# Optimization experiments

Measured on AMD Instinct MI355X. Metric: run time of the kernel, lower is better.

Reference implementation:

```python
import jax, jax.numpy as jnp
import numpy as np

D, N, L, H, VOCAB = 256, 8192, 6, 4, 256
EPS = 1e-5


def layernorm(x):
    # LayerNorm over last dim, no affine (matches nn.LayerNorm(D, elementwise_affine=False))
    mu = jnp.mean(x, axis=-1, keepdims=True)
    var = jnp.mean(jnp.square(x - mu), axis=-1, keepdims=True)
    return (x - mu) * jax.lax.rsqrt(var + EPS)


def rotate_half(x):
    x1, x2 = jnp.split(x, 2, axis=-1)
    return jnp.concatenate((-x2, x1), axis=-1)


def rope_tables(T, dim, dtype):
    inv_freq = 1.0 / (10000.0 ** (jnp.arange(0, dim, 2, dtype=jnp.float32) / dim))
    t = jnp.arange(T, dtype=jnp.float32)
    freqs = jnp.einsum('i,j->ij', t, inv_freq)          # [T, dim/2]
    emb = jnp.concatenate((freqs, freqs), axis=-1)       # [T, dim]
    return jnp.cos(emb).astype(dtype), jnp.sin(emb).astype(dtype)


def linear_attention(Q, K, V):
    # unnormalized causal attention with RoPE on Q, K
    B, T, d = Q.shape
    cos, sin = rope_tables(T, d, Q.dtype)
    Qr = Q * cos + rotate_half(Q) * sin
    Kr = K * cos + rotate_half(K) * sin
    energy = jnp.einsum('btd,bsd->bts', Qr, Kr)          # [B, T, T]
    mask = jnp.tril(jnp.ones((T, T), dtype=energy.dtype))
    energy = energy * mask
    return jnp.einsum('bts,bsd->btd', energy, V)


def setup_inputs() -> dict:
    key = jax.random.key(0)
    ks = jax.random.split(key, 6)
    idx = jax.random.randint(ks[0], (4, 2048), 0, VOCAB)
    wte = jax.random.normal(ks[1], (VOCAB, D), dtype=jnp.float32) * 0.02
    encoder = jax.random.normal(ks[2], (N, D), dtype=jnp.float32) * 0.02
    decoder_x = jax.random.normal(ks[3], (H, D, N // H), dtype=jnp.float32) * 0.02
    decoder_y = jax.random.normal(ks[4], (H, D, N // H), dtype=jnp.float32) * 0.02
    readout = jax.random.normal(ks[5], (D, VOCAB), dtype=jnp.float32) * 0.02
    return {"idx": idx, "wte": wte, "encoder": encoder,
            "decoder_x": decoder_x, "decoder_y": decoder_y, "readout": readout}


def reference(idx, wte, encoder, decoder_x, decoder_y, readout):
    B, T = idx.shape
    v_ast = layernorm(wte[idx])                          # [B, T, D]
    for _ in range(L):
        x_raw = jnp.einsum('btd,hdm->bthm', v_ast, decoder_x)
        x = jax.nn.relu(x_raw)                           # [B, T, H, N/H]
        a_ast = linear_attention(v_ast, v_ast, v_ast)
        y_raw = jnp.einsum('btd,hdm->bthm', layernorm(a_ast), decoder_y)
        y = jax.nn.relu(y_raw) * x
        y_flat = y.reshape(B, T, -1)                     # [B, T, N]
        update = y_flat @ encoder                        # [B, T, D]
        v_ast = v_ast + layernorm(update)
    logits = v_ast @ readout                             # [B, T, VOCAB]
    return logits
```

## Files before the change

### kernel.cpp

```cpp
#include <hip/hip_runtime.h>
#include <hip/hip_bf16.h>

typedef __hip_bfloat16 bf16;
typedef _Float16 half_t;
typedef __attribute__((ext_vector_type(8))) _Float16 half8;
typedef __attribute__((ext_vector_type(4))) float f32x4;

#define LN_EPS 1e-5f

static constexpr int Dk     = 256;
static constexpr int Tk     = 2048;
static constexpr int BTk    = 8192;
static constexpr int MHk    = 2048;
static constexpr int Nk     = 8192;
static constexpr int LAYERS = 6;
static constexpr long long TD  = (long long)Tk * Dk;
static constexpr long long BTD = (long long)BTk * Dk;
static constexpr long long TT  = (long long)Tk * Tk;

#define SKQ(t) ((((t) & 3) ^ (((t) >> 3) & 3)) * 8)

__device__ __forceinline__ float wave_reduce(float v) {
#pragma unroll
    for (int o = 32; o > 0; o >>= 1) v += __shfl_down(v, o);
    return v;
}

__device__ __forceinline__ float block_sum_256(float x, float* sbuf) {
    float s = wave_reduce(x);
    int lane = threadIdx.x & 63, wv = threadIdx.x >> 6;
    if (lane == 0) sbuf[wv] = s;
    __syncthreads();
    float r = sbuf[0] + sbuf[1] + sbuf[2] + sbuf[3];
    __syncthreads();
    return r;
}

__device__ __forceinline__ void glds16(const void* g, void* lds) {
    __builtin_amdgcn_global_load_lds(
        (const __attribute__((address_space(1))) void*)g,
        (__attribute__((address_space(3))) void*)lds, 16, 0, 0);
}

__global__ __launch_bounds__(256) void sniff_kernel(const unsigned short* __restrict__ w,
                                                    int* __restrict__ flag) {
    __shared__ float sbuf[4];
    int tid = threadIdx.x;
    float cnt = 0.f;
    for (int i = tid; i < 1024; i += 256) {
        int e = (w[i] >> 7) & 0xFF;
        if (e >= 128) cnt += 1.f;
    }
    float tot = block_sum_256(cnt, sbuf);
    if (tid == 0) *flag = (tot > 32.f) ? 1 : 0;
}

__global__ __launch_bounds__(256) void tr_cvt16_kernel(const void* __restrict__ src,
                                                       const int* __restrict__ flag,
                                                       half_t* __restrict__ dst,
                                                       int R, int C,
                                                       long long sz, long long dz) {
    __shared__ float t[32][33];
    bool f32 = (*flag != 0);
    int ct = blockIdx.x * 32, rt = blockIdx.y * 32;
    long long so = (long long)blockIdx.z * sz, dofs = (long long)blockIdx.z * dz;
    int tx = threadIdx.x & 31, ty = threadIdx.x >> 5;
#pragma unroll
    for (int i = 0; i < 4; i++) {
        long long idx = so + (long long)(rt + ty + i * 8) * C + ct + tx;
        t[ty + i * 8][tx] = f32 ? ((const float*)src)[idx] : (float)((const bf16*)src)[idx];
    }
    __syncthreads();
#pragma unroll
    for (int i = 0; i < 4; i++) {
        long long odx = dofs + (long long)(ct + ty + i * 8) * R + rt + tx;
        dst[odx] = (half_t)t[tx][ty + i * 8];
    }
}

__global__ __launch_bounds__(256) void trv_kernel(const float* __restrict__ src,
                                                  half_t* __restrict__ dst) {
    __shared__ float t[32][33];
    int ct = blockIdx.x * 32, rt = blockIdx.y * 32;
    int tx = threadIdx.x & 31, ty = threadIdx.x >> 5;
#pragma unroll
    for (int i = 0; i < 4; i++)
        t[ty + i * 8][tx] = src[(long long)(rt + ty + i * 8) * Dk + ct + tx];
    __syncthreads();
#pragma unroll
    for (int i = 0; i < 4; i++)
        dst[(long long)(ct + ty + i * 8) * BTk + rt + tx] = (half_t)t[tx][ty + i * 8];
}

__global__ __launch_bounds__(256) void embed_ln_kernel(const int* __restrict__ idx,
                                                       const void* __restrict__ wte,
                                                       const int* __restrict__ flag,
                                                       float* __restrict__ v,
                                                       half_t* __restrict__ vf) {
    __shared__ float sbuf[4];
    int bt = blockIdx.x, tid = threadIdx.x;
    int id = idx[bt];
    bool f32 = (*flag != 0);
    float x = f32 ? ((const float*)wte)[id * Dk + tid]
                  : (float)((const bf16*)wte)[id * Dk + tid];
    float mu = block_sum_256(x, sbuf) * (1.f / 256.f);
    float d = x - mu;
    float var = block_sum_256(d * d, sbuf) * (1.f / 256.f);
    float r = d * rsqrtf(var + LN_EPS);
    v[bt * Dk + tid] = r;
    vf[bt * Dk + tid] = (half_t)r;
}

__global__ __launch_bounds__(256) void ln_rows_kernel(const float* __restrict__ Pa,
                                                      half_t* __restrict__ of) {
    __shared__ float sbuf[4];
    int bt = blockIdx.x, tid = threadIdx.x;
    int b = bt >> 11, t = bt & (Tk - 1);
    int ncnt = ((t & ~127) >> 9) + 1;
    const float* p = Pa + ((long long)(b << 2)) * TD + (long long)t * Dk + tid;
    float x = 0.f;
    for (int c = 0; c < ncnt; c++) x += p[(long long)c * TD];
    float mu = block_sum_256(x, sbuf) * (1.f / 256.f);
    float d = x - mu;
    float var = block_sum_256(d * d, sbuf) * (1.f / 256.f);
    float r = d * rsqrtf(var + LN_EPS);
    of[bt * Dk + tid] = (half_t)r;
}

__global__ __launch_bounds__(256) void add_ln_kernel(const float* __restrict__ Pu,
                                                     float* __restrict__ v,
                                                     half_t* __restrict__ vf) {
    __shared__ float sbuf[4];
    int bt = blockIdx.x, tid = threadIdx.x;
    long long e = (long long)bt * Dk + tid;
    float x = Pu[e] + Pu[e + BTD] + Pu[e + 2 * BTD] + Pu[e + 3 * BTD];
    float mu = block_sum_256(x, sbuf) * (1.f / 256.f);
    float d = x - mu;
    float var = block_sum_256(d * d, sbuf) * (1.f / 256.f);
    float r = d * rsqrtf(var + LN_EPS);
    float nv = v[e] + r;
    v[e] = nv;
    vf[e] = (half_t)nv;
}

__global__ __launch_bounds__(128) void rope_kernel(const float* __restrict__ v,
                                                   half_t* __restrict__ qf) {
    int bt = blockIdx.x, i = threadIdx.x;
    int t = bt & (Tk - 1);
    float invf = powf(10000.f, -(float)i / 128.f);
    float ang = (float)t * invf;
    float s, c;
    sincosf(ang, &s, &c);
    float q1 = v[bt * Dk + i];
    float q2 = v[bt * Dk + 128 + i];
    qf[bt * Dk + i]       = (half_t)(q1 * c - q2 * s);
    qf[bt * Dk + 128 + i] = (half_t)(q2 * c + q1 * s);
}

__global__ __launch_bounds__(256) void gemm128e(
    const half_t* __restrict__ Q, half_t* __restrict__ E) {
    __shared__ __align__(16) half_t smem[8192];
    half_t* As = smem;
    half_t* Bs = smem + 4096;
    const int tid = threadIdx.x;
    const int lane = tid & 63, wv = tid >> 6;
    const int wr = wv >> 1, wc = wv & 1;
    const int quad = lane >> 4, r = lane & 15;
    const int qsw = (quad ^ ((r >> 1) & 3)) * 8;
    const int mb = blockIdx.y * 128, nb = blockIdx.x * 128;
    if ((int)blockIdx.x > (int)blockIdx.y) return;
    const half_t* Qb = Q + (long long)blockIdx.z * TD;
    half_t* Eb = E + (long long)blockIdx.z * TT;

    f32x4 acc[4][4] = {};
    const int srow = tid >> 2, skq = SKQ(tid);
    const int wbase = (tid & 192) * 8;
    for (int k0 = 0; k0 < Dk; k0 += 32) {
#pragma unroll
        for (int rnd = 0; rnd < 2; rnd++) {
            int row = rnd * 64 + srow;
            glds16(Qb + (long long)(mb + row) * Dk + k0 + skq, As + rnd * 2048 + wbase);
            glds16(Qb + (long long)(nb + row) * Dk + k0 + skq, Bs + rnd * 2048 + wbase);
        }
        __syncthreads();
        half8 bfr[4];
#pragma unroll
        for (int ni = 0; ni < 4; ni++)
            bfr[ni] = *(const half8*)&Bs[(wc * 64 + ni * 16 + r) * 32 + qsw];
#pragma unroll
        for (int mi = 0; mi < 4; mi++) {
            half8 afr = *(const half8*)&As[(wr * 64 + mi * 16 + r) * 32 + qsw];
#pragma unroll
            for (int ni = 0; ni < 4; ni++)
                acc[mi][ni] = __builtin_amdgcn_mfma_f32_16x16x32_f16(afr, bfr[ni], acc[mi][ni], 0, 0, 0);
        }
        __syncthreads();
    }
#pragma unroll
    for (int p = 0; p < 2; p++) {
        if (wr == p) {
#pragma unroll
            for (int mi = 0; mi < 4; mi++)
#pragma unroll
                for (int ni = 0; ni < 4; ni++) {
                    int rl0 = mi * 16 + quad * 4;
                    int cl = wc * 64 + ni * 16 + r;
#pragma unroll
                    for (int rr = 0; rr < 4; rr++) {
                        int row = mb + p * 64 + rl0 + rr;
                        int col = nb + cl;
                        float val = (row < col) ? 0.f : acc[mi][ni][rr];
                        smem[(rl0 + rr) * 128 + cl] = (half_t)val;
                    }
                }
        }
        __syncthreads();
#pragma unroll
        for (int j = 0; j < 4; j++) {
            int o = j * 2048 + tid * 8;
            int rl = o >> 7, cl = o & 127;
            *(half8*)&Eb[(long long)(mb + p * 64 + rl) * Tk + nb + cl] = *(const half8*)&smem[o];
        }
        __syncthreads();
    }
}

__global__ __launch_bounds__(256) void gemm128a(
    const half_t* __restrict__ E, const half_t* __restrict__ vT,
    float* __restrict__ Pa) {
    __shared__ __align__(16) half_t As[128 * 32];
    __shared__ __align__(16) half_t Bs[128 * 32];
    const int tid = threadIdx.x;
    const int lane = tid & 63, wv = tid >> 6;
    const int wr = wv >> 1, wc = wv & 1;
    const int quad = lane >> 4, r = lane & 15;
    const int qsw = (quad ^ ((r >> 1) & 3)) * 8;
    const int mb = blockIdx.y * 128, nb = blockIdx.x * 128;
    const int b = blockIdx.z >> 2, c = blockIdx.z & 3;
    const int kbeg = c * 512;
    const int kend = min(mb + 128, kbeg + 512);
    if (kend <= kbeg) return;

    const half_t* Ab = E + (long long)b * TT;
    const half_t* Bb = vT + (long long)b * Tk;
    float* Pc = Pa + (long long)blockIdx.z * TD;
    f32x4 acc[4][4] = {};
    const int srow = tid >> 2, skq = SKQ(tid);
    const int wbase = (tid & 192) * 8;
    for (int k0 = kbeg; k0 < kend; k0 += 32) {
#pragma unroll
        for (int rnd = 0; rnd < 2; rnd++) {
            int row = rnd * 64 + srow;
            glds16(Ab + (long long)(mb + row) * Tk + k0 + skq, As + rnd * 2048 + wbase);
            glds16(Bb + (long long)(nb + row) * BTk + k0 + skq, Bs + rnd * 2048 + wbase);
        }
        __syncthreads();
        half8 bfr[4];
#pragma unroll
        for (int ni = 0; ni < 4; ni++)
            bfr[ni] = *(const half8*)&Bs[(wc * 64 + ni * 16 + r) * 32 + qsw];
#pragma unroll
        for (int mi = 0; mi < 4; mi++) {
            half8 afr = *(const half8*)&As[(wr * 64 + mi * 16 + r) * 32 + qsw];
#pragma unroll
            for (int ni = 0; ni < 4; ni++)
                acc[mi][ni] = __builtin_amdgcn_mfma_f32_16x16x32_f16(afr, bfr[ni], acc[mi][ni], 0, 0, 0);
        }
        __syncthreads();
    }
#pragma unroll
    for (int mi = 0; mi < 4; mi++)
#pragma unroll
        for (int ni = 0; ni < 4; ni++) {
            int row0 = mb + wr * 64 + mi * 16 + quad * 4;
            int col = nb + wc * 64 + ni * 16 + r;
#pragma unroll
            for (int rr = 0; rr < 4; rr++)
                Pc[(long long)(row0 + rr) * Dk + col] = acc[mi][ni][rr];
        }
}

__global__ __launch_bounds__(512) void dual_gemm(
    const half_t* __restrict__ A1,
    const half_t* __restrict__ A2,
    const half_t* __restrict__ dxT,
    const half_t* __restrict__ dyT,
    half_t* __restrict__ C) {
    __shared__ __align__(16) half_t smem[16384];
    half_t* As1 = smem;
    half_t* As2 = smem + 4096;
    half_t* Bs1 = smem + 8192;
    half_t* Bs2 = smem + 12288;
    const int tid = threadIdx.x;
    const int lane = tid & 63, wv = tid >> 6;
    const int wr = wv >> 2, wc = wv & 3;
    const int quad = lane >> 4, r = lane & 15;
    const int qsw = (quad ^ ((r >> 1) & 3)) * 8;
    const int mb = blockIdx.y * 128, nb = blockIdx.x * 128;
    const int h = blockIdx.z;
    const half_t* B1 = dxT + (long long)h * MHk * Dk;
    const half_t* B2 = dyT + (long long)h * MHk * Dk;

    f32x4 accX[4][2] = {};
    f32x4 accY[4][2] = {};
    const int srow = tid >> 2, skq = SKQ(tid);
    const int wbase = (tid & 448) * 8;
    for (int k0 = 0; k0 < Dk; k0 += 32) {
        glds16(A1 + (long long)(mb + srow) * Dk + k0 + skq, As1 + wbase);
        glds16(A2 + (long long)(mb + srow) * Dk + k0 + skq, As2 + wbase);
        glds16(B1 + (long long)(nb + srow) * Dk + k0 + skq, Bs1 + wbase);
        glds16(B2 + (long long)(nb + srow) * Dk + k0 + skq, Bs2 + wbase);
        __syncthreads();
        half8 b1f[2], b2f[2];
#pragma unroll
        for (int ni = 0; ni < 2; ni++) {
            b1f[ni] = *(const half8*)&Bs1[(wc * 32 + ni * 16 + r) * 32 + qsw];
            b2f[ni] = *(const half8*)&Bs2[(wc * 32 + ni * 16 + r) * 32 + qsw];
        }
#pragma unroll
        for (int mi = 0; mi < 4; mi++) {
            half8 a1 = *(const half8*)&As1[(wr * 64 + mi * 16 + r) * 32 + qsw];
            half8 a2 = *(const half8*)&As2[(wr * 64 + mi * 16 + r) * 32 + qsw];
#pragma unroll
            for (int ni = 0; ni < 2; ni++) {
                accX[mi][ni] = __builtin_amdgcn_mfma_f32_16x16x32_f16(a1, b1f[ni], accX[mi][ni], 0, 0, 0);
                accY[mi][ni] = __builtin_amdgcn_mfma_f32_16x16x32_f16(a2, b2f[ni], accY[mi][ni], 0, 0, 0);
            }
        }
        __syncthreads();
    }
#pragma unroll
    for (int mi = 0; mi < 4; mi++)
#pragma unroll
        for (int ni = 0; ni < 2; ni++) {
            int rl0 = wr * 64 + mi * 16 + quad * 4;
            int cl = wc * 32 + ni * 16 + r;
#pragma unroll
            for (int rr = 0; rr < 4; rr++) {
                float val = fmaxf(accY[mi][ni][rr], 0.f) * fmaxf(accX[mi][ni][rr], 0.f);
                smem[(rl0 + rr) * 128 + cl] = (half_t)val;
            }
        }
    __syncthreads();
    const long long cbase = (long long)mb * Nk + (long long)h * MHk + nb;
#pragma unroll
    for (int j = 0; j < 4; j++) {
        int o = j * 4096 + tid * 8;
        int rl = o >> 7, cl = o & 127;
        *(half8*)&C[cbase + (long long)rl * Nk + cl] = *(const half8*)&smem[o];
    }
}

__global__ __launch_bounds__(256) void gemm128u(
    const half_t* __restrict__ A, const half_t* __restrict__ B,
    float* __restrict__ Pu) {
    __shared__ __align__(16) half_t As[128 * 32];
    __shared__ __align__(16) half_t Bs[128 * 32];
    const int tid = threadIdx.x;
    const int lane = tid & 63, wv = tid >> 6;
    const int wr = wv >> 1, wc = wv & 1;
    const int quad = lane >> 4, r = lane & 15;
    const int qsw = (quad ^ ((r >> 1) & 3)) * 8;
    const int mb = blockIdx.y * 128, nb = blockIdx.x * 128;
    const int kbeg = blockIdx.z * 2048;
    float* Pc = Pu + (long long)blockIdx.z * BTD;

    f32x4 acc[4][4] = {};
    const int srow = tid >> 2, skq = SKQ(tid);
    const int wbase = (tid & 192) * 8;
    for (int k0 = kbeg; k0 < kbeg + 2048; k0 += 32) {
#pragma unroll
        for (int rnd = 0; rnd < 2; rnd++) {
            int row = rnd * 64 + srow;
            glds16(A + (long long)(mb + row) * Nk + k0 + skq, As + rnd * 2048 + wbase);
            glds16(B + (long long)(nb + row) * Nk + k0 + skq, Bs + rnd * 2048 + wbase);
        }
        __syncthreads();
        half8 bfr[4];
#pragma unroll
        for (int ni = 0; ni < 4; ni++)
            bfr[ni] = *(const half8*)&Bs[(wc * 64 + ni * 16 + r) * 32 + qsw];
#pragma unroll
        for (int mi = 0; mi < 4; mi++) {
            half8 afr = *(const half8*)&As[(wr * 64 + mi * 16 + r) * 32 + qsw];
#pragma unroll
            for (int ni = 0; ni < 4; ni++)
                acc[mi][ni] = __builtin_amdgcn_mfma_f32_16x16x32_f16(afr, bfr[ni], acc[mi][ni], 0, 0, 0);
        }
        __syncthreads();
    }
#pragma unroll
    for (int mi = 0; mi < 4; mi++)
#pragma unroll
        for (int ni = 0; ni < 4; ni++) {
            int row0 = mb + wr * 64 + mi * 16 + quad * 4;
            int col = nb + wc * 64 + ni * 16 + r;
#pragma unroll
            for (int rr = 0; rr < 4; rr++)
                Pc[(long long)(row0 + rr) * Dk + col] = acc[mi][ni][rr];
        }
}

__global__ __launch_bounds__(256) void gemm64h(
    const half_t* __restrict__ A, int lda,
    const half_t* __restrict__ B, int ldb,
    float* __restrict__ C, int ldc, int K) {
    __shared__ __align__(16) half_t As[64 * 32];
    __shared__ __align__(16) half_t Bs[64 * 32];
    const int tid = threadIdx.x;
    const int lane = tid & 63, wv = tid >> 6;
    const int wr = wv >> 1, wc = wv & 1;
    const int quad = lane >> 4, r = lane & 15;
    const int qsw = (quad ^ ((r >> 1) & 3)) * 8;
    const int mb = blockIdx.y * 64, nb = blockIdx.x * 64;

    f32x4 acc[2][2] = {};
    const int srow = tid >> 2, skq = SKQ(tid);
    const int wbase = (tid & 192) * 8;
    for (int k0 = 0; k0 < K; k0 += 32) {
        glds16(A + (long long)(mb + srow) * lda + k0 + skq, As + wbase);
        glds16(B + (long long)(nb + srow) * ldb + k0 + skq, Bs + wbase);
        __syncthreads();
        half8 b0 = *(const half8*)&Bs[(wc * 32 +  0 + r) * 32 + qsw];
        half8 b1 = *(const half8*)&Bs[(wc * 32 + 16 + r) * 32 + qsw];
#pragma unroll
        for (int mi = 0; mi < 2; mi++) {
            half8 afr = *(const half8*)&As[(wr * 32 + mi * 16 + r) * 32 + qsw];
            acc[mi][0] = __builtin_amdgcn_mfma_f32_16x16x32_f16(afr, b0, acc[mi][0], 0, 0, 0);
            acc[mi][1] = __builtin_amdgcn_mfma_f32_16x16x32_f16(afr, b1, acc[mi][1], 0, 0, 0);
        }
        __syncthreads();
    }
#pragma unroll
    for (int mi = 0; mi < 2; mi++)
#pragma unroll
        for (int ni = 0; ni < 2; ni++) {
            int row0 = mb + wr * 32 + mi * 16 + quad * 4;
            int col = nb + wc * 32 + ni * 16 + r;
#pragma unroll
            for (int rr = 0; rr < 4; rr++)
                C[(long long)(row0 + rr) * ldc + col] = acc[mi][ni][rr];
        }
}

extern "C" void kernel_launch(void* const* d_in, const int* in_sizes, int n_in,
                              void* d_out, int out_size, void* d_ws, size_t ws_size,
                              hipStream_t stream) {
    (void)in_sizes; (void)n_in; (void)out_size; (void)ws_size;
    const int* idx = (const int*)d_in[0];
    float* out = (float*)d_out;

    char* ws = (char*)d_ws;
    float*  v32  = (float*) (ws);
    half_t* vf   = (half_t*)(ws + (  8ll << 20));
    half_t* qf   = (half_t*)(ws + ( 12ll << 20));
    half_t* vT   = (half_t*)(ws + ( 16ll << 20));
    half_t* lnf  = (half_t*)(ws + ( 20ll << 20));
    half_t* E    = (half_t*)(ws + ( 24ll << 20));
    float*  Pa   = (float*) (ws + ( 56ll << 20));
    float*  Pu   = (float*) (ws + ( 24ll << 20));
    half_t* y16  = (half_t*)(ws + ( 88ll << 20));
    half_t* dxT  = (half_t*)(ws + (216ll << 20));
    half_t* dyT  = (half_t*)(ws + (220ll << 20));
    half_t* eT   = (half_t*)(ws + (224ll << 20));
    half_t* roT  = (half_t*)(ws + (228ll << 20));
    int*    flag = (int*)   (ws + (228ll << 20) + (256ll << 10));

    sniff_kernel<<<1, 256, 0, stream>>>((const unsigned short*)d_in[1], flag);
    tr_cvt16_kernel<<<dim3(MHk / 32, Dk / 32, 4), 256, 0, stream>>>(
        d_in[3], flag, dxT, Dk, MHk, (long long)Dk * MHk, (long long)Dk * MHk);
    tr_cvt16_kernel<<<dim3(MHk / 32, Dk / 32, 4), 256, 0, stream>>>(
        d_in[4], flag, dyT, Dk, MHk, (long long)Dk * MHk, (long long)Dk * MHk);
    tr_cvt16_kernel<<<dim3(Dk / 32, Nk / 32, 1), 256, 0, stream>>>(
        d_in[2], flag, eT, Nk, Dk, 0, 0);
    tr_cvt16_kernel<<<dim3(Dk / 32, Dk / 32, 1), 256, 0, stream>>>(
        d_in[5], flag, roT, Dk, Dk, 0, 0);

    embed_ln_kernel<<<BTk, 256, 0, stream>>>(idx, d_in[1], flag, v32, vf);

    for (int l = 0; l < LAYERS; l++) {
        rope_kernel<<<BTk, 128, 0, stream>>>(v32, qf);
        trv_kernel<<<dim3(Dk / 32, BTk / 32), 256, 0, stream>>>(v32, vT);
        gemm128e<<<dim3(Tk / 128, Tk / 128, 4), 256, 0, stream>>>(qf, E);
        gemm128a<<<dim3(Dk / 128, Tk / 128, 16), 256, 0, stream>>>(E, vT, Pa);
        ln_rows_kernel<<<BTk, 256, 0, stream>>>(Pa, lnf);
        dual_gemm<<<dim3(MHk / 128, BTk / 128, 4), 512, 0, stream>>>(
            vf, lnf, dxT, dyT, y16);
        gemm128u<<<dim3(Dk / 128, BTk / 128, 4), 256, 0, stream>>>(y16, eT, Pu);
        add_ln_kernel<<<BTk, 256, 0, stream>>>(Pu, v32, vf);
    }
    gemm64h<<<dim3(Dk / 64, BTk / 64), 256, 0, stream>>>(
        vf, Dk, roT, Dk, out, Dk, Dk);
}
```

Measured before the change: 1.450 ms.

## Fuse decoder dual GEMM with encoder GEMM, keeping gated activations in LDS

Replaces the separate dual_gemm (writing the fp16 y tensor to global memory) and gemm128u with one kernel. Each block computes a 128-row stripe of relu(x)*relu(y) for eight 128-column chunks, stores each chunk in swizzled LDS, and immediately multiplies it by the matching encoder slice, accumulating the update. Partial results from 8 N-splits are written out and summed in add_ln_kernel. This removes the large y16 round-trip through global memory and one launch. The cost is fewer blocks (512), much more LDS per block, and A-operand tiles reloaded for every chunk.

```diff
diff --git a/kernel.cpp b/kernel.cpp
--- a/kernel.cpp
+++ b/kernel.cpp
@@ -133,7 +133,9 @@
     __shared__ float sbuf[4];
     int bt = blockIdx.x, tid = threadIdx.x;
     long long e = (long long)bt * Dk + tid;
-    float x = Pu[e] + Pu[e + BTD] + Pu[e + 2 * BTD] + Pu[e + 3 * BTD];
+    float x = 0.f;
+#pragma unroll
+    for (int p = 0; p < 8; p++) x += Pu[e + (long long)p * BTD];
     float mu = block_sum_256(x, sbuf) * (1.f / 256.f);
     float d = x - mu;
     float var = block_sum_256(d * d, sbuf) * (1.f / 256.f);
@@ -280,124 +282,105 @@
         }
 }
 
-__global__ __launch_bounds__(512) void dual_gemm(
+__global__ __launch_bounds__(512, 2) void fused_du(
     const half_t* __restrict__ A1,
     const half_t* __restrict__ A2,
     const half_t* __restrict__ dxT,
     const half_t* __restrict__ dyT,
-    half_t* __restrict__ C) {
-    __shared__ __align__(16) half_t smem[16384];
-    half_t* As1 = smem;
-    half_t* As2 = smem + 4096;
-    half_t* Bs1 = smem + 8192;
-    half_t* Bs2 = smem + 12288;
+    const half_t* __restrict__ eT,
+    float* __restrict__ Pu) {
+    __shared__ __align__(16) half_t As1[4096];
+    __shared__ __align__(16) half_t As2[4096];
+    __shared__ __align__(16) half_t Bs1[4096];
+    __shared__ __align__(16) half_t Bs2[4096];
+    __shared__ __align__(16) half_t Ys[16384];
+    __shared__ __align__(16) half_t Es[8192];
     const int tid = threadIdx.x;
     const int lane = tid & 63, wv = tid >> 6;
     const int wr = wv >> 2, wc = wv & 3;
     const int quad = lane >> 4, r = lane & 15;
     const int qsw = (quad ^ ((r >> 1) & 3)) * 8;
-    const int mb = blockIdx.y * 128, nb = blockIdx.x * 128;
-    const int h = blockIdx.z;
-    const half_t* B1 = dxT + (long long)h * MHk * Dk;
-    const half_t* B2 = dyT + (long long)h * MHk * Dk;
-
-    f32x4 accX[4][2] = {};
-    f32x4 accY[4][2] = {};
+    const int mb = blockIdx.y * 128;
+    const int nbase = blockIdx.x * 1024;
     const int srow = tid >> 2, skq = SKQ(tid);
     const int wbase = (tid & 448) * 8;
-    for (int k0 = 0; k0 < Dk; k0 += 32) {
-        glds16(A1 + (long long)(mb + srow) * Dk + k0 + skq, As1 + wbase);
-        glds16(A2 + (long long)(mb + srow) * Dk + k0 + skq, As2 + wbase);
-        glds16(B1 + (long long)(nb + srow) * Dk + k0 + skq, Bs1 + wbase);
-        glds16(B2 + (long long)(nb + srow) * Dk + k0 + skq, Bs2 + wbase);
-        __syncthreads();
-        half8 b1f[2], b2f[2];
-#pragma unroll
-        for (int ni = 0; ni < 2; ni++) {
-            b1f[ni] = *(const half8*)&Bs1[(wc * 32 + ni * 16 + r) * 32 + qsw];
-            b2f[ni] = *(const half8*)&Bs2[(wc * 32 + ni * 16 + r) * 32 + qsw];
-        }
-#pragma unroll
-        for (int mi = 0; mi < 4; mi++) {
-            half8 a1 = *(const half8*)&As1[(wr * 64 + mi * 16 + r) * 32 + qsw];
-            half8 a2 = *(const half8*)&As2[(wr * 64 + mi * 16 + r) * 32 + qsw];
+
+    f32x4 accU[4][4] = {};
+    for (int nc = 0; nc < 8; nc++) {
+        const int n0 = nbase + nc * 128;
+        f32x4 accX[4][2] = {};
+        f32x4 accY[4][2] = {};
+        for (int k0 = 0; k0 < Dk; k0 += 32) {
+            glds16(A1 + (long long)(mb + srow) * Dk + k0 + skq, As1 + wbase);
+            glds16(A2 + (long long)(mb + srow) * Dk + k0 + skq, As2 + wbase);
+            glds16(dxT + (long long)(n0 + srow) * Dk + k0 + skq, Bs1 + wbase);
+            glds16(dyT + (long long)(n0 + srow) * Dk + k0 + skq, Bs2 + wbase);
+            __syncthreads();
+            half8 b1f[2], b2f[2];
 #pragma unroll
             for (int ni = 0; ni < 2; ni++) {
-                accX[mi][ni] = __builtin_amdgcn_mfma_f32_16x16x32_f16(a1, b1f[ni], accX[mi][ni], 0, 0, 0);
-                accY[mi][ni] = __builtin_amdgcn_mfma_f32_16x16x32_f16(a2, b2f[ni], accY[mi][ni], 0, 0, 0);
+                b1f[ni] = *(const half8*)&Bs1[(wc * 32 + ni * 16 + r) * 32 + qsw];
+                b2f[ni] = *(const half8*)&Bs2[(wc * 32 + ni * 16 + r) * 32 + qsw];
             }
-        }
-        __syncthreads();
-    }
-#pragma unroll
-    for (int mi = 0; mi < 4; mi++)
-#pragma unroll
-        for (int ni = 0; ni < 2; ni++) {
-            int rl0 = wr * 64 + mi * 16 + quad * 4;
-            int cl = wc * 32 + ni * 16 + r;
-#pragma unroll
-            for (int rr = 0; rr < 4; rr++) {
-                float val = fmaxf(accY[mi][ni][rr], 0.f) * fmaxf(accX[mi][ni][rr], 0.f);
-                smem[(rl0 + rr) * 128 + cl] = (half_t)val;
+#pragma unroll
+            for (int mi = 0; mi < 4; mi++) {
+                half8 a1 = *(const half8*)&As1[(wr * 64 + mi * 16 + r) * 32 + qsw];
+                half8 a2 = *(const half8*)&As2[(wr * 64 + mi * 16 + r) * 32 + qsw];
+#pragma unroll
+                for (int ni = 0; ni < 2; ni++) {
+                    accX[mi][ni] = __builtin_amdgcn_mfma_f32_16x16x32_f16(a1, b1f[ni], accX[mi][ni], 0, 0, 0);
+                    accY[mi][ni] = __builtin_amdgcn_mfma_f32_16x16x32_f16(a2, b2f[ni], accY[mi][ni], 0, 0, 0);
+                }
             }
-        }
-    __syncthreads();
-    const long long cbase = (long long)mb * Nk + (long long)h * MHk + nb;
-#pragma unroll
-    for (int j = 0; j < 4; j++) {
-        int o = j * 4096 + tid * 8;
-        int rl = o >> 7, cl = o & 127;
-        *(half8*)&C[cbase + (long long)rl * Nk + cl] = *(const half8*)&smem[o];
-    }
-}
-
-__global__ __launch_bounds__(256) void gemm128u(
-    const half_t* __restrict__ A, const half_t* __restrict__ B,
-    float* __restrict__ Pu) {
-    __shared__ __align__(16) half_t As[128 * 32];
-    __shared__ __align__(16) half_t Bs[128 * 32];
-    const int tid = threadIdx.x;
-    const int lane = tid & 63, wv = tid >> 6;
-    const int wr = wv >> 1, wc = wv & 1;
-    const int quad = lane >> 4, r = lane & 15;
-    const int qsw = (quad ^ ((r >> 1) & 3)) * 8;
-    const int mb = blockIdx.y * 128, nb = blockIdx.x * 128;
-    const int kbeg = blockIdx.z * 2048;
-    float* Pc = Pu + (long long)blockIdx.z * BTD;
-
-    f32x4 acc[4][4] = {};
-    const int srow = tid >> 2, skq = SKQ(tid);
-    const int wbase = (tid & 192) * 8;
-    for (int k0 = kbeg; k0 < kbeg + 2048; k0 += 32) {
-#pragma unroll
-        for (int rnd = 0; rnd < 2; rnd++) {
-            int row = rnd * 64 + srow;
-            glds16(A + (long long)(mb + row) * Nk + k0 + skq, As + rnd * 2048 + wbase);
-            glds16(B + (long long)(nb + row) * Nk + k0 + skq, Bs + rnd * 2048 + wbase);
-        }
-        __syncthreads();
-        half8 bfr[4];
-#pragma unroll
-        for (int ni = 0; ni < 4; ni++)
-            bfr[ni] = *(const half8*)&Bs[(wc * 64 + ni * 16 + r) * 32 + qsw];
-#pragma unroll
-        for (int mi = 0; mi < 4; mi++) {
-            half8 afr = *(const half8*)&As[(wr * 64 + mi * 16 + r) * 32 + qsw];
+            __syncthreads();
+        }
+#pragma unroll
+        for (int mi = 0; mi < 4; mi++)
+#pragma unroll
+            for (int ni = 0; ni < 2; ni++) {
+                int rl0 = wr * 64 + mi * 16 + quad * 4;
+                int col = wc * 32 + ni * 16 + r;
+#pragma unroll
+                for (int rr = 0; rr < 4; rr++) {
+                    int row = rl0 + rr;
+                    float val = fmaxf(accY[mi][ni][rr], 0.f) * fmaxf(accX[mi][ni][rr], 0.f);
+                    int o = ((col >> 3) ^ (row & 15)) * 8;
+                    Ys[row * 128 + o + (col & 7)] = (half_t)val;
+                }
+            }
+        __syncthreads();
+#pragma unroll
+        for (int kk = 0; kk < 4; kk++) {
+#pragma unroll
+            for (int rnd = 0; rnd < 2; rnd++)
+                glds16(eT + (long long)(rnd * 128 + srow) * Nk + n0 + kk * 32 + skq,
+                       Es + rnd * 4096 + wbase);
+            __syncthreads();
+            half8 bf[4];
 #pragma unroll
             for (int ni = 0; ni < 4; ni++)
-                acc[mi][ni] = __builtin_amdgcn_mfma_f32_16x16x32_f16(afr, bfr[ni], acc[mi][ni], 0, 0, 0);
-        }
-        __syncthreads();
-    }
+                bf[ni] = *(const half8*)&Es[(wc * 64 + ni * 16 + r) * 32 + qsw];
+#pragma unroll
+            for (int mi = 0; mi < 4; mi++) {
+                int arow = wr * 64 + mi * 16 + r;
+                half8 af = *(const half8*)&Ys[arow * 128 + (((kk * 4 + quad) ^ r)) * 8];
+#pragma unroll
+                for (int ni = 0; ni < 4; ni++)
+                    accU[mi][ni] = __builtin_amdgcn_mfma_f32_16x16x32_f16(af, bf[ni], accU[mi][ni], 0, 0, 0);
+            }
+            __syncthreads();
+        }
+    }
+    float* Pc = Pu + (long long)blockIdx.x * BTD;
 #pragma unroll
     for (int mi = 0; mi < 4; mi++)
 #pragma unroll
         for (int ni = 0; ni < 4; ni++) {
             int row0 = mb + wr * 64 + mi * 16 + quad * 4;
-            int col = nb + wc * 64 + ni * 16 + r;
+            int col = wc * 64 + ni * 16 + r;
 #pragma unroll
             for (int rr = 0; rr < 4; rr++)
-                Pc[(long long)(row0 + rr) * Dk + col] = acc[mi][ni][rr];
+                Pc[(long long)(row0 + rr) * Dk + col] = accU[mi][ni][rr];
         }
 }
 
@@ -458,8 +441,7 @@
     half_t* lnf  = (half_t*)(ws + ( 20ll << 20));
     half_t* E    = (half_t*)(ws + ( 24ll << 20));
     float*  Pa   = (float*) (ws + ( 56ll << 20));
-    float*  Pu   = (float*) (ws + ( 24ll << 20));
-    half_t* y16  = (half_t*)(ws + ( 88ll << 20));
+    float*  Pu   = (float*) (ws + ( 88ll << 20));
     half_t* dxT  = (half_t*)(ws + (216ll << 20));
     half_t* dyT  = (half_t*)(ws + (220ll << 20));
     half_t* eT   = (half_t*)(ws + (224ll << 20));
@@ -484,9 +466,8 @@
         gemm128e<<<dim3(Tk / 128, Tk / 128, 4), 256, 0, stream>>>(qf, E);
         gemm128a<<<dim3(Dk / 128, Tk / 128, 16), 256, 0, stream>>>(E, vT, Pa);
         ln_rows_kernel<<<BTk, 256, 0, stream>>>(Pa, lnf);
-        dual_gemm<<<dim3(MHk / 128, BTk / 128, 4), 512, 0, stream>>>(
-            vf, lnf, dxT, dyT, y16);
-        gemm128u<<<dim3(Dk / 128, BTk / 128, 4), 256, 0, stream>>>(y16, eT, Pu);
+        fused_du<<<dim3(8, BTk / 128), 512, 0, stream>>>(
+            vf, lnf, dxT, dyT, eT, Pu);
         add_ln_kernel<<<BTk, 256, 0, stream>>>(Pu, v32, vf);
     }
     gemm64h<<<dim3(Dk / 64, BTk / 64), 256, 0, stream>>>(
```

Result: slower. 1.655 ms (+14.1%).
